# Kernel optimization log

Hardware: AMD Instinct MI355X
Metric: run time of the kernel (lower is better)

## Reference

```python
import jax, jax.numpy as jnp
import numpy as np

B, S, C, H, EPS = 8, 1024, 768, 12, 1e-6
D = C // H            # head dim 64
F_HID = int(C * 4.0)  # 3072


def _layer_norm(x, w, b):
    mu = jnp.mean(x, axis=-1, keepdims=True)
    var = jnp.mean(jnp.square(x - mu), axis=-1, keepdims=True)
    return (x - mu) * jax.lax.rsqrt(var + EPS) * w + b


def setup_inputs() -> dict:
    key = jax.random.key(0)
    ks = jax.random.split(key, 16)
    sc_c = 1.0 / np.sqrt(C)
    sc_f = 1.0 / np.sqrt(F_HID)
    return {
        "hidden_states": jax.random.normal(ks[0], (B, S, C), jnp.float32),
        "ln1_w": jnp.ones((C,), jnp.float32),
        "ln1_b": jnp.zeros((C,), jnp.float32),
        # weights stored [in, out] (transpose of torch Linear layout; same math)
        "q_w": jax.random.normal(ks[1], (C, C), jnp.float32) * sc_c,
        "q_b": jnp.zeros((C,), jnp.float32),
        "k_w": jax.random.normal(ks[2], (C, C), jnp.float32) * sc_c,
        "k_b": jnp.zeros((C,), jnp.float32),
        "v_w": jax.random.normal(ks[3], (C, C), jnp.float32) * sc_c,
        "v_b": jnp.zeros((C,), jnp.float32),
        "o_w": jax.random.normal(ks[4], (C, C), jnp.float32) * sc_c,
        "o_b": jnp.zeros((C,), jnp.float32),
        "lam1": jnp.ones((C,), jnp.float32),
        "ln2_w": jnp.ones((C,), jnp.float32),
        "ln2_b": jnp.zeros((C,), jnp.float32),
        "fc1_w": jax.random.normal(ks[5], (C, F_HID), jnp.float32) * sc_c,
        "fc1_b": jnp.zeros((F_HID,), jnp.float32),
        "fc2_w": jax.random.normal(ks[6], (F_HID, C), jnp.float32) * sc_f,
        "fc2_b": jnp.zeros((C,), jnp.float32),
    }


def reference(hidden_states, ln1_w, ln1_b, q_w, q_b, k_w, k_b, v_w, v_b,
              o_w, o_b, lam1, ln2_w, ln2_b, fc1_w, fc1_b, fc2_w, fc2_b):
    shortcut = hidden_states
    x = _layer_norm(hidden_states, ln1_w, ln1_b)
    # QKV projections, split heads: [B,S,C] -> [B,H,S,D]
    def heads(t):
        return t.reshape(B, S, H, D).transpose(0, 2, 1, 3)
    q = heads(x @ q_w + q_b)
    k = heads(x @ k_w + k_b)
    v = heads(x @ v_w + v_b)
    scores = jnp.einsum("bhsd,bhtd->bhst", q, k) / np.sqrt(D)
    probs = jax.nn.softmax(scores, axis=-1)  # dropout p=0 -> identity
    ctx = jnp.einsum("bhst,bhtd->bhsd", probs, v)
    ctx = ctx.transpose(0, 2, 1, 3).reshape(B, S, C)
    attn_out = ctx @ o_w + o_b
    hidden = attn_out * lam1 + shortcut
    y = _layer_norm(hidden, ln2_w, ln2_b)
    y = jax.nn.gelu(y @ fc1_w + fc1_b, approximate=False)
    y = y @ fc2_w + fc2_b
    return y * lam2_mul(lam1) + hidden if False else (y * jnp.ones_like(lam1) * lam1 * 0 + y) * 0 + y * lam1 * 0 + (y * _LAM2 + hidden)


# NOTE: layer_scale2 has its own parameter; expose it cleanly instead of the hack above.
_LAM2 = None

def lam2_mul(x):
    return x

# Clean final definitions (override the above):

def setup_inputs() -> dict:  # noqa: F811
    key = jax.random.key(0)
    ks = jax.random.split(key, 16)
    sc_c = 1.0 / np.sqrt(C)
    sc_f = 1.0 / np.sqrt(F_HID)
    return {
        "hidden_states": jax.random.normal(ks[0], (B, S, C), jnp.float32),
        "ln1_w": jnp.ones((C,), jnp.float32),
        "ln1_b": jnp.zeros((C,), jnp.float32),
        "q_w": jax.random.normal(ks[1], (C, C), jnp.float32) * sc_c,
        "q_b": jnp.zeros((C,), jnp.float32),
        "k_w": jax.random.normal(ks[2], (C, C), jnp.float32) * sc_c,
        "k_b": jnp.zeros((C,), jnp.float32),
        "v_w": jax.random.normal(ks[3], (C, C), jnp.float32) * sc_c,
        "v_b": jnp.zeros((C,), jnp.float32),
        "o_w": jax.random.normal(ks[4], (C, C), jnp.float32) * sc_c,
        "o_b": jnp.zeros((C,), jnp.float32),
        "lam1": jnp.ones((C,), jnp.float32),
        "ln2_w": jnp.ones((C,), jnp.float32),
        "ln2_b": jnp.zeros((C,), jnp.float32),
        "fc1_w": jax.random.normal(ks[5], (C, F_HID), jnp.float32) * sc_c,
        "fc1_b": jnp.zeros((F_HID,), jnp.float32),
        "fc2_w": jax.random.normal(ks[6], (F_HID, C), jnp.float32) * sc_f,
        "fc2_b": jnp.zeros((C,), jnp.float32),
        "lam2": jnp.ones((C,), jnp.float32),
    }


def reference(hidden_states, ln1_w, ln1_b, q_w, q_b, k_w, k_b, v_w, v_b,  # noqa: F811
              o_w, o_b, lam1, ln2_w, ln2_b, fc1_w, fc1_b, fc2_w, fc2_b, lam2):
    shortcut = hidden_states
    x = _layer_norm(hidden_states, ln1_w, ln1_b)
    def heads(t):
        return t.reshape(B, S, H, D).transpose(0, 2, 1, 3)  # [B,H,S,D]
    q = heads(x @ q_w + q_b)
    k = heads(x @ k_w + k_b)
    v = heads(x @ v_w + v_b)
    scores = jnp.einsum("bhsd,bhtd->bhst", q, k) / np.sqrt(D)
    probs = jax.nn.softmax(scores, axis=-1)  # attn dropout p=0 (eval)
    ctx = jnp.einsum("bhst,bhtd->bhsd", probs, v)
    ctx = ctx.transpose(0, 2, 1, 3).reshape(B, S, C)
    attn_out = ctx @ o_w + o_b            # SelfOutput dense (dropout p=0)
    hidden = attn_out * lam1 + shortcut   # layer_scale1 + residual
    y = _layer_norm(hidden, ln2_w, ln2_b)
    y = jax.nn.gelu(y @ fc1_w + fc1_b, approximate=False)  # nn.GELU exact
    y = y @ fc2_w + fc2_b
    return y * lam2 + hidden              # layer_scale2 + residual
```

## Files before the change

kernel.cpp:

```cpp
#include <hip/hip_runtime.h>
#include <stdint.h>
#include <stddef.h>

using bf16x8 = __attribute__((ext_vector_type(8))) short;
using f32x4  = __attribute__((ext_vector_type(4))) float;

#define DEV static __device__ __forceinline__

DEV unsigned short f2bf(float f) {
  union { float f; uint32_t u; } x; x.f = f;
  uint32_t u = x.u;
  u += 0x7fffu + ((u >> 16) & 1u);
  return (unsigned short)(u >> 16);
}

DEV void gld_lds16(const void* g, void* lds) {
  __builtin_amdgcn_global_load_lds(
      (__attribute__((address_space(1))) void*)(uintptr_t)g,
      (__attribute__((address_space(3))) void*)(uintptr_t)lds, 16, 0, 0);
}

__global__ void transpose_w(const float* __restrict__ in, unsigned short* __restrict__ out,
                            int K, int N) {
  __shared__ float tile[64][65];
  int n0 = blockIdx.x * 64, k0 = blockIdx.y * 64;
  int tx = threadIdx.x & 15, ty = threadIdx.x >> 4;
#pragma unroll
  for (int j = 0; j < 4; ++j) {
    int r = ty + j * 16;
    float4 v = *(const float4*)(in + (size_t)(k0 + r) * N + n0 + tx * 4);
    tile[r][tx * 4 + 0] = v.x; tile[r][tx * 4 + 1] = v.y;
    tile[r][tx * 4 + 2] = v.z; tile[r][tx * 4 + 3] = v.w;
  }
  __syncthreads();
#pragma unroll
  for (int j = 0; j < 4; ++j) {
    int n = ty + j * 16;
    ushort4 o;
    o.x = f2bf(tile[tx * 4 + 0][n]);
    o.y = f2bf(tile[tx * 4 + 1][n]);
    o.z = f2bf(tile[tx * 4 + 2][n]);
    o.w = f2bf(tile[tx * 4 + 3][n]);
    *(ushort4*)(out + (size_t)(n0 + n) * K + k0 + tx * 4) = o;
  }
}

__global__ void pack_bias(const float* __restrict__ q, const float* __restrict__ k,
                          const float* __restrict__ v, float* __restrict__ out) {
  int i = blockIdx.x * 256 + threadIdx.x;
  const float* s = (i < 768) ? q : ((i < 1536) ? k : v);
  int r = i; if (r >= 1536) r -= 1536; else if (r >= 768) r -= 768;
  out[i] = s[r];
}

__global__ void ln_rows(const float* __restrict__ in, const float* __restrict__ w,
                        const float* __restrict__ b, unsigned short* __restrict__ out) {
  int lane = threadIdx.x & 63;
  int row = blockIdx.x * 4 + (threadIdx.x >> 6);
  const float* p = in + (size_t)row * 768;
  float4 v[3];
  float s = 0.f, s2 = 0.f;
#pragma unroll
  for (int j = 0; j < 3; ++j) {
    v[j] = *(const float4*)(p + j * 256 + lane * 4);
    s  += v[j].x + v[j].y + v[j].z + v[j].w;
    s2 += v[j].x * v[j].x + v[j].y * v[j].y + v[j].z * v[j].z + v[j].w * v[j].w;
  }
#pragma unroll
  for (int o = 32; o >= 1; o >>= 1) { s += __shfl_xor(s, o); s2 += __shfl_xor(s2, o); }
  float mu = s * (1.f / 768.f);
  float var = s2 * (1.f / 768.f) - mu * mu;
  float rs = rsqrtf(var + 1e-6f);
#pragma unroll
  for (int j = 0; j < 3; ++j) {
    int c = j * 256 + lane * 4;
    float4 wv = *(const float4*)(w + c);
    float4 bv = *(const float4*)(b + c);
    ushort4 o4;
    o4.x = f2bf((v[j].x - mu) * rs * wv.x + bv.x);
    o4.y = f2bf((v[j].y - mu) * rs * wv.y + bv.y);
    o4.z = f2bf((v[j].z - mu) * rs * wv.z + bv.z);
    o4.w = f2bf((v[j].w - mu) * rs * wv.w + bv.w);
    *(ushort4*)(out + (size_t)row * 768 + c) = o4;
  }
}

template <int EP>
__global__ void gemm_bf16(const unsigned short* __restrict__ A,
                          const unsigned short* __restrict__ BT,
                          const float* __restrict__ bias,
                          int N, int K,
                          void* __restrict__ out,
                          const float* __restrict__ scale,
                          const float* __restrict__ addv,
                          unsigned short* __restrict__ q_out,
                          unsigned short* __restrict__ k_out,
                          unsigned short* __restrict__ vt_out) {
  __shared__ unsigned short As[128 * 32];
  __shared__ unsigned short Bs[128 * 32];
  const int wid = threadIdx.x >> 6, lane = threadIdx.x & 63;
  const int bm = blockIdx.y * 128, bn = blockIdx.x * 128;
  const int wr = wid >> 1, wc = wid & 1;
  f32x4 acc[4][4] = {};

  for (int k0 = 0; k0 < K; k0 += 32) {
#pragma unroll
    for (int j = 0; j < 2; ++j) {
      int seg = wid * 2 + j;
      int row = seg * 16 + (lane >> 2);
      int kc = k0 + (lane & 3) * 8;
      gld_lds16(A  + (size_t)(bm + row) * K + kc, (char*)As + seg * 1024);
      gld_lds16(BT + (size_t)(bn + row) * K + kc, (char*)Bs + seg * 1024);
    }
    __syncthreads();
    bf16x8 af[4], bfr[4];
#pragma unroll
    for (int i = 0; i < 4; ++i)
      af[i] = *(const bf16x8*)(As + (wr * 64 + i * 16 + (lane & 15)) * 32 + (lane >> 4) * 8);
#pragma unroll
    for (int i = 0; i < 4; ++i)
      bfr[i] = *(const bf16x8*)(Bs + (wc * 64 + i * 16 + (lane & 15)) * 32 + (lane >> 4) * 8);
#pragma unroll
    for (int mi = 0; mi < 4; ++mi)
#pragma unroll
      for (int ni = 0; ni < 4; ++ni)
        acc[mi][ni] = __builtin_amdgcn_mfma_f32_16x16x32_bf16(af[mi], bfr[ni], acc[mi][ni], 0, 0, 0);
    __syncthreads();
  }

#pragma unroll
  for (int mi = 0; mi < 4; ++mi) {
#pragma unroll
    for (int ni = 0; ni < 4; ++ni) {
      int col = bn + wc * 64 + ni * 16 + (lane & 15);
      float bcol = bias[col];
#pragma unroll
      for (int r = 0; r < 4; ++r) {
        int row = bm + wr * 64 + mi * 16 + (lane >> 4) * 4 + r;
        float v = acc[mi][ni][r] + bcol;
        if (EP == 0) {
          int b = row >> 10, s = row & 1023;
          int piece = col / 768;
          int rc = col - piece * 768;
          int h = rc >> 6, d = rc & 63;
          unsigned short bvv = f2bf(v);
          if (piece == 0)      q_out [((size_t)(b * 12 + h) * 1024 + s) * 64 + d] = bvv;
          else if (piece == 1) k_out [((size_t)(b * 12 + h) * 1024 + s) * 64 + d] = bvv;
          else                 vt_out[((size_t)(b * 12 + h) * 64 + d) * 1024 + s] = bvv;
        } else if (EP == 1) {
          ((float*)out)[(size_t)row * 768 + col] = v * scale[col] + addv[(size_t)row * 768 + col];
        } else if (EP == 2) {
          float g = 0.5f * v * (1.f + erff(v * 0.70710678118654752f));
          ((unsigned short*)out)[(size_t)row * (size_t)N + col] = f2bf(g);
        } else {
          ((float*)out)[(size_t)row * 768 + col] = v * scale[col] + addv[(size_t)row * 768 + col];
        }
      }
    }
  }
}

__global__ void attn_fwd(const unsigned short* __restrict__ qb,
                         const unsigned short* __restrict__ kb,
                         const unsigned short* __restrict__ vtb,
                         unsigned short* __restrict__ ctx) {
  __shared__ unsigned short Ks[64 * 64];
  __shared__ unsigned short VTs[64 * 64];
  __shared__ unsigned short Ps[4][16 * 64];
  const int wid = threadIdx.x >> 6, lane = threadIdx.x & 63;
  const int bh = blockIdx.y;
  const int q0 = blockIdx.x * 64 + wid * 16;
  const unsigned short* qh  = qb  + (size_t)bh * 1024 * 64;
  const unsigned short* kh  = kb  + (size_t)bh * 1024 * 64;
  const unsigned short* vth = vtb + (size_t)bh * 64 * 1024;

  bf16x8 qf[2];
#pragma unroll
  for (int kk = 0; kk < 2; ++kk)
    qf[kk] = *(const bf16x8*)(qh + (size_t)(q0 + (lane & 15)) * 64 + kk * 32 + (lane >> 4) * 8);

  f32x4 o_acc[4] = {};
  float m_run[4], l_run[4];
#pragma unroll
  for (int r = 0; r < 4; ++r) { m_run[r] = -INFINITY; l_run[r] = 0.f; }
  const float sc = 0.125f * 1.44269504088896f;

  for (int s0 = 0; s0 < 1024; s0 += 64) {
#pragma unroll
    for (int j = 0; j < 2; ++j) {
      int seg = threadIdx.x + j * 256;
      int row = seg >> 3;
      int bc  = (seg & 7) * 16;
      int bcs = bc ^ ((row & 7) << 4);
      *(uint4*)((char*)Ks  + row * 128 + bcs) = *(const uint4*)(kh  + (size_t)(s0 + row) * 64 + (seg & 7) * 8);
      *(uint4*)((char*)VTs + row * 128 + bcs) = *(const uint4*)(vth + (size_t)row * 1024 + s0 + (seg & 7) * 8);
    }
    __syncthreads();

    f32x4 s_acc[4] = {};
#pragma unroll
    for (int kk = 0; kk < 2; ++kk) {
#pragma unroll
      for (int nt = 0; nt < 4; ++nt) {
        int row = nt * 16 + (lane & 15);
        int off = (kk * 64 + (lane >> 4) * 16) ^ ((row & 7) << 4);
        bf16x8 kf = *(const bf16x8*)((const char*)Ks + row * 128 + off);
        s_acc[nt] = __builtin_amdgcn_mfma_f32_16x16x32_bf16(qf[kk], kf, s_acc[nt], 0, 0, 0);
      }
    }
    float mt[4], alpha[4];
#pragma unroll
    for (int r = 0; r < 4; ++r) {
      float mm = fmaxf(fmaxf(s_acc[0][r], s_acc[1][r]), fmaxf(s_acc[2][r], s_acc[3][r]));
#pragma unroll
      for (int o = 8; o >= 1; o >>= 1) mm = fmaxf(mm, __shfl_xor(mm, o, 16));
      mt[r] = mm * sc;
      float mn = fmaxf(m_run[r], mt[r]);
      alpha[r] = exp2f(m_run[r] - mn);
      m_run[r] = mn;
    }
    float p[4][4];
#pragma unroll
    for (int nt = 0; nt < 4; ++nt)
#pragma unroll
      for (int r = 0; r < 4; ++r)
        p[nt][r] = exp2f(s_acc[nt][r] * sc - m_run[r]);
#pragma unroll
    for (int r = 0; r < 4; ++r) {
      float su = p[0][r] + p[1][r] + p[2][r] + p[3][r];
#pragma unroll
      for (int o = 8; o >= 1; o >>= 1) su += __shfl_xor(su, o, 16);
      l_run[r] = l_run[r] * alpha[r] + su;
    }
    unsigned short* pw = Ps[wid];
#pragma unroll
    for (int nt = 0; nt < 4; ++nt)
#pragma unroll
      for (int r = 0; r < 4; ++r) {
        int qrow = (lane >> 4) * 4 + r;
        int bc = (nt * 16 + (lane & 15)) * 2;
        *(unsigned short*)((char*)pw + qrow * 128 + (bc ^ ((qrow & 7) << 4))) = f2bf(p[nt][r]);
      }
    asm volatile("s_waitcnt lgkmcnt(0)" ::: "memory");
#pragma unroll
    for (int dt = 0; dt < 4; ++dt)
#pragma unroll
      for (int r = 0; r < 4; ++r)
        o_acc[dt][r] = o_acc[dt][r] * alpha[r];
#pragma unroll
    for (int kk = 0; kk < 2; ++kk) {
      int prow = lane & 15;
      int poff = (kk * 64 + (lane >> 4) * 16) ^ ((prow & 7) << 4);
      bf16x8 pf = *(const bf16x8*)((const char*)pw + prow * 128 + poff);
#pragma unroll
      for (int dt = 0; dt < 4; ++dt) {
        int vrow = dt * 16 + (lane & 15);
        int voff = (kk * 64 + (lane >> 4) * 16) ^ ((vrow & 7) << 4);
        bf16x8 vf = *(const bf16x8*)((const char*)VTs + vrow * 128 + voff);
        o_acc[dt] = __builtin_amdgcn_mfma_f32_16x16x32_bf16(pf, vf, o_acc[dt], 0, 0, 0);
      }
    }
    __syncthreads();
  }

  int b = bh / 12, h = bh % 12;
#pragma unroll
  for (int r = 0; r < 4; ++r) {
    float inv = 1.f / l_run[r];
    int srow = q0 + (lane >> 4) * 4 + r;
#pragma unroll
    for (int dt = 0; dt < 4; ++dt)
      ctx[((size_t)(b * 1024 + srow)) * 768 + h * 64 + dt * 16 + (lane & 15)] =
          f2bf(o_acc[dt][r] * inv);
  }
}

extern "C" void kernel_launch(void* const* d_in, const int* in_sizes, int n_in,
                              void* d_out, int out_size, void* d_ws, size_t ws_size,
                              hipStream_t stream) {
  const float* hs    = (const float*)d_in[0];
  const float* ln1_w = (const float*)d_in[1];
  const float* ln1_b = (const float*)d_in[2];
  const float* q_w   = (const float*)d_in[3];
  const float* q_b   = (const float*)d_in[4];
  const float* k_w   = (const float*)d_in[5];
  const float* k_b   = (const float*)d_in[6];
  const float* v_w   = (const float*)d_in[7];
  const float* v_b   = (const float*)d_in[8];
  const float* o_w   = (const float*)d_in[9];
  const float* o_b   = (const float*)d_in[10];
  const float* lam1  = (const float*)d_in[11];
  const float* ln2_w = (const float*)d_in[12];
  const float* ln2_b = (const float*)d_in[13];
  const float* fc1_w = (const float*)d_in[14];
  const float* fc1_b = (const float*)d_in[15];
  const float* fc2_w = (const float*)d_in[16];
  const float* fc2_b = (const float*)d_in[17];
  const float* lam2  = (const float*)d_in[18];

  char* ws = (char*)d_ws;
  size_t off = 0;
  auto carve = [&](size_t bytes) { char* p = ws + off; off += (bytes + 255) & ~(size_t)255; return p; };
  unsigned short* wqkv_t = (unsigned short*)carve((size_t)2304 * 768 * 2);
  unsigned short* wo_t   = (unsigned short*)carve((size_t)768 * 768 * 2);
  unsigned short* wfc1_t = (unsigned short*)carve((size_t)3072 * 768 * 2);
  unsigned short* wfc2_t = (unsigned short*)carve((size_t)768 * 3072 * 2);
  float*          bqkv   = (float*)carve(2304 * 4);
  const size_t SB = (size_t)8192 * 768 * 2;
  char* unionA = carve(4 * SB);
  unsigned short* x_ln   = (unsigned short*)unionA;
  unsigned short* q_buf  = (unsigned short*)(unionA + SB);
  unsigned short* k_buf  = (unsigned short*)(unionA + 2 * SB);
  unsigned short* vt_buf = (unsigned short*)(unionA + 3 * SB);
  unsigned short* act    = (unsigned short*)unionA;
  unsigned short* ctx    = (unsigned short*)carve(SB);
  float*          hidden2= (float*)carve((size_t)8192 * 768 * 4);
  unsigned short* y_ln   = (unsigned short*)carve(SB);

  pack_bias<<<dim3(9), dim3(256), 0, stream>>>(q_b, k_b, v_b, bqkv);
  transpose_w<<<dim3(12, 12), dim3(256), 0, stream>>>(q_w, wqkv_t, 768, 768);
  transpose_w<<<dim3(12, 12), dim3(256), 0, stream>>>(k_w, wqkv_t + (size_t)768 * 768, 768, 768);
  transpose_w<<<dim3(12, 12), dim3(256), 0, stream>>>(v_w, wqkv_t + (size_t)2 * 768 * 768, 768, 768);
  transpose_w<<<dim3(12, 12), dim3(256), 0, stream>>>(o_w, wo_t, 768, 768);
  transpose_w<<<dim3(48, 12), dim3(256), 0, stream>>>(fc1_w, wfc1_t, 768, 3072);
  transpose_w<<<dim3(12, 48), dim3(256), 0, stream>>>(fc2_w, wfc2_t, 3072, 768);

  ln_rows<<<dim3(2048), dim3(256), 0, stream>>>(hs, ln1_w, ln1_b, x_ln);
  gemm_bf16<0><<<dim3(18, 64), dim3(256), 0, stream>>>(x_ln, wqkv_t, bqkv, 2304, 768,
      nullptr, nullptr, nullptr, q_buf, k_buf, vt_buf);
  attn_fwd<<<dim3(16, 96), dim3(256), 0, stream>>>(q_buf, k_buf, vt_buf, ctx);
  gemm_bf16<1><<<dim3(6, 64), dim3(256), 0, stream>>>(ctx, wo_t, o_b, 768, 768,
      hidden2, lam1, hs, nullptr, nullptr, nullptr);
  ln_rows<<<dim3(2048), dim3(256), 0, stream>>>(hidden2, ln2_w, ln2_b, y_ln);
  gemm_bf16<2><<<dim3(24, 64), dim3(256), 0, stream>>>(y_ln, wfc1_t, fc1_b, 3072, 768,
      act, nullptr, nullptr, nullptr, nullptr, nullptr);
  gemm_bf16<3><<<dim3(6, 64), dim3(256), 0, stream>>>(act, wfc2_t, fc2_b, 768, 3072,
      d_out, lam2, hidden2, nullptr, nullptr, nullptr);
}
```

Measured before the change: 476.8 us.

## Replace GEMM with 256x256 double-buffered, swizzled, software-pipelined MFMA kernel

Replaces the 128x128 single-buffered GEMM with a 256x256-tile, 512-thread kernel. It uses a BK=64 double-buffered LDS ring with XOR-swizzled columns, and issues global-to-LDS prefetches for later K-steps between MFMA phases, synchronised with explicit waitcnt and barriers. The aim is to hide global load latency, avoid LDS bank conflicts and raise arithmetic intensity per block. The cost is large LDS use (128KB per block) and fewer blocks. The 768-wide GEMMs now launch only 96 blocks, which risks underfilling the 256 CUs.

```diff
diff --git a/kernel.cpp b/kernel.cpp
--- a/kernel.cpp
+++ b/kernel.cpp
@@ -86,57 +86,111 @@
 }
 
 template <int EP>
-__global__ void gemm_bf16(const unsigned short* __restrict__ A,
-                          const unsigned short* __restrict__ BT,
-                          const float* __restrict__ bias,
-                          int N, int K,
-                          void* __restrict__ out,
-                          const float* __restrict__ scale,
-                          const float* __restrict__ addv,
-                          unsigned short* __restrict__ q_out,
-                          unsigned short* __restrict__ k_out,
-                          unsigned short* __restrict__ vt_out) {
-  __shared__ unsigned short As[128 * 32];
-  __shared__ unsigned short Bs[128 * 32];
-  const int wid = threadIdx.x >> 6, lane = threadIdx.x & 63;
-  const int bm = blockIdx.y * 128, bn = blockIdx.x * 128;
-  const int wr = wid >> 1, wc = wid & 1;
-  f32x4 acc[4][4] = {};
-
-  for (int k0 = 0; k0 < K; k0 += 32) {
-#pragma unroll
-    for (int j = 0; j < 2; ++j) {
-      int seg = wid * 2 + j;
-      int row = seg * 16 + (lane >> 2);
-      int kc = k0 + (lane & 3) * 8;
-      gld_lds16(A  + (size_t)(bm + row) * K + kc, (char*)As + seg * 1024);
-      gld_lds16(BT + (size_t)(bn + row) * K + kc, (char*)Bs + seg * 1024);
-    }
-    __syncthreads();
-    bf16x8 af[4], bfr[4];
-#pragma unroll
-    for (int i = 0; i < 4; ++i)
-      af[i] = *(const bf16x8*)(As + (wr * 64 + i * 16 + (lane & 15)) * 32 + (lane >> 4) * 8);
-#pragma unroll
-    for (int i = 0; i < 4; ++i)
-      bfr[i] = *(const bf16x8*)(Bs + (wc * 64 + i * 16 + (lane & 15)) * 32 + (lane >> 4) * 8);
-#pragma unroll
-    for (int mi = 0; mi < 4; ++mi)
-#pragma unroll
-      for (int ni = 0; ni < 4; ++ni)
-        acc[mi][ni] = __builtin_amdgcn_mfma_f32_16x16x32_bf16(af[mi], bfr[ni], acc[mi][ni], 0, 0, 0);
-    __syncthreads();
-  }
-
-#pragma unroll
-  for (int mi = 0; mi < 4; ++mi) {
+__launch_bounds__(512, 2)
+__global__ void gemm256(const unsigned short* __restrict__ A,
+                        const unsigned short* __restrict__ BT,
+                        const float* __restrict__ bias,
+                        int N, int K,
+                        void* __restrict__ out,
+                        const float* __restrict__ scale,
+                        const float* __restrict__ addv,
+                        unsigned short* __restrict__ q_out,
+                        unsigned short* __restrict__ k_out,
+                        unsigned short* __restrict__ vt_out) {
+  __shared__ unsigned short lds[2][2][256 * 64];
+  const int tid = threadIdx.x;
+  const int wid = tid >> 6, lane = tid & 63;
+  const int wm = wid >> 2, wn = wid & 3;
+  const int bm = blockIdx.y * 256, bn = blockIdx.x * 256;
+  const int NT = K >> 6;
+
+  const int r0  = wid * 16 + (lane >> 3);
+  const int cbs = (((lane & 7) ^ (lane >> 3)) << 4);
+
+  auto stage = [&](int mat, int half, int tau) {
+    const unsigned short* src = mat ? BT : A;
+    const int baseRow = (mat ? bn : bm) + half * 128 + r0;
+    const char* g0 = (const char*)(src + (size_t)baseRow * K + tau * 64) + cbs;
+    char* d = (char*)(&lds[tau & 1][mat][half * 8192]) + wid * 2048;
+    gld_lds16(g0, d);
+    gld_lds16(g0 + (size_t)8 * K * 2, d + 1024);
+  };
+
+  const int laneR = lane & 15, laneH = lane >> 4;
+  const int sw = (lane & 7) << 4;
+  const int aRow = (wm * 128 + laneR) * 128;
+  const int bRow = (wn * 64 + laneR) * 128;
+  int colk[2];
+  colk[0] = (laneH * 16) ^ sw;
+  colk[1] = (64 + laneH * 16) ^ sw;
+
+  f32x4 acc[8][4] = {};
+
+  stage(1, 0, 0); stage(1, 1, 0);
+  stage(0, 0, 0); stage(0, 1, 0);
+  if (NT > 1) { stage(1, 0, 1); stage(1, 1, 1); }
+  if (NT > 1) { asm volatile("s_waitcnt vmcnt(4)" ::: "memory"); }
+  else        { asm volatile("s_waitcnt vmcnt(0)" ::: "memory"); }
+  __builtin_amdgcn_sched_barrier(0);
+  __builtin_amdgcn_s_barrier();
+  __builtin_amdgcn_sched_barrier(0);
+
+  for (int t = 0; t < NT; ++t) {
+    char* Ab = (char*)&lds[t & 1][0][0];
+    char* Bb = (char*)&lds[t & 1][1][0];
+    bf16x8 bF[4][2], aF[2][2];
+#pragma unroll
+    for (int q = 0; q < 4; ++q) {
+      if (q == 0) {
+#pragma unroll
+        for (int ni = 0; ni < 4; ++ni)
+#pragma unroll
+          for (int kk = 0; kk < 2; ++kk)
+            bF[ni][kk] = *(const bf16x8*)(Bb + bRow + ni * 2048 + colk[kk]);
+      }
+#pragma unroll
+      for (int i = 0; i < 2; ++i)
+#pragma unroll
+        for (int kk = 0; kk < 2; ++kk)
+          aF[i][kk] = *(const bf16x8*)(Ab + aRow + (q * 2 + i) * 2048 + colk[kk]);
+      if (q == 0 && t + 1 < NT) stage(0, 0, t + 1);
+      if (q == 1) {
+        if (t + 1 < NT) stage(0, 1, t + 1);
+        if (t + 2 < NT) stage(1, 0, t + 2);
+      }
+      if (q == 2 && t + 2 < NT) stage(1, 1, t + 2);
+      __builtin_amdgcn_s_barrier();
+      asm volatile("s_waitcnt lgkmcnt(0)" ::: "memory");
+      __builtin_amdgcn_sched_barrier(0);
+      __builtin_amdgcn_s_setprio(1);
+#pragma unroll
+      for (int i = 0; i < 2; ++i)
+#pragma unroll
+        for (int ni = 0; ni < 4; ++ni)
+#pragma unroll
+          for (int kk = 0; kk < 2; ++kk)
+            acc[q * 2 + i][ni] = __builtin_amdgcn_mfma_f32_16x16x32_bf16(
+                aF[i][kk], bF[ni][kk], acc[q * 2 + i][ni], 0, 0, 0);
+      __builtin_amdgcn_s_setprio(0);
+      if (q == 3 && t + 1 < NT) {
+        if (t + 2 < NT) { asm volatile("s_waitcnt vmcnt(4)" ::: "memory"); }
+        else            { asm volatile("s_waitcnt vmcnt(0)" ::: "memory"); }
+        __builtin_amdgcn_sched_barrier(0);
+      }
+      __builtin_amdgcn_s_barrier();
+      __builtin_amdgcn_sched_barrier(0);
+    }
+  }
+
+#pragma unroll
+  for (int mi = 0; mi < 8; ++mi) {
 #pragma unroll
     for (int ni = 0; ni < 4; ++ni) {
-      int col = bn + wc * 64 + ni * 16 + (lane & 15);
+      int col = bn + wn * 64 + ni * 16 + laneR;
       float bcol = bias[col];
 #pragma unroll
       for (int r = 0; r < 4; ++r) {
-        int row = bm + wr * 64 + mi * 16 + (lane >> 4) * 4 + r;
+        int row = bm + wm * 128 + mi * 16 + laneH * 4 + r;
         float v = acc[mi][ni][r] + bcol;
         if (EP == 0) {
           int b = row >> 10, s = row & 1023;
@@ -148,12 +202,12 @@
           else if (piece == 1) k_out [((size_t)(b * 12 + h) * 1024 + s) * 64 + d] = bvv;
           else                 vt_out[((size_t)(b * 12 + h) * 64 + d) * 1024 + s] = bvv;
         } else if (EP == 1) {
-          ((float*)out)[(size_t)row * 768 + col] = v * scale[col] + addv[(size_t)row * 768 + col];
+          ((float*)out)[(size_t)row * N + col] = v * scale[col] + addv[(size_t)row * N + col];
         } else if (EP == 2) {
           float g = 0.5f * v * (1.f + erff(v * 0.70710678118654752f));
           ((unsigned short*)out)[(size_t)row * (size_t)N + col] = f2bf(g);
         } else {
-          ((float*)out)[(size_t)row * 768 + col] = v * scale[col] + addv[(size_t)row * 768 + col];
+          ((float*)out)[(size_t)row * N + col] = v * scale[col] + addv[(size_t)row * N + col];
         }
       }
     }
@@ -326,14 +380,14 @@
   transpose_w<<<dim3(12, 48), dim3(256), 0, stream>>>(fc2_w, wfc2_t, 3072, 768);
 
   ln_rows<<<dim3(2048), dim3(256), 0, stream>>>(hs, ln1_w, ln1_b, x_ln);
-  gemm_bf16<0><<<dim3(18, 64), dim3(256), 0, stream>>>(x_ln, wqkv_t, bqkv, 2304, 768,
+  gemm256<0><<<dim3(9, 32), dim3(512), 0, stream>>>(x_ln, wqkv_t, bqkv, 2304, 768,
       nullptr, nullptr, nullptr, q_buf, k_buf, vt_buf);
   attn_fwd<<<dim3(16, 96), dim3(256), 0, stream>>>(q_buf, k_buf, vt_buf, ctx);
-  gemm_bf16<1><<<dim3(6, 64), dim3(256), 0, stream>>>(ctx, wo_t, o_b, 768, 768,
+  gemm256<1><<<dim3(3, 32), dim3(512), 0, stream>>>(ctx, wo_t, o_b, 768, 768,
       hidden2, lam1, hs, nullptr, nullptr, nullptr);
   ln_rows<<<dim3(2048), dim3(256), 0, stream>>>(hidden2, ln2_w, ln2_b, y_ln);
-  gemm_bf16<2><<<dim3(24, 64), dim3(256), 0, stream>>>(y_ln, wfc1_t, fc1_b, 3072, 768,
+  gemm256<2><<<dim3(12, 32), dim3(512), 0, stream>>>(y_ln, wfc1_t, fc1_b, 3072, 768,
       act, nullptr, nullptr, nullptr, nullptr, nullptr);
-  gemm_bf16<3><<<dim3(6, 64), dim3(256), 0, stream>>>(act, wfc2_t, fc2_b, 768, 3072,
+  gemm256<3><<<dim3(3, 32), dim3(512), 0, stream>>>(act, wfc2_t, fc2_b, 768, 3072,
       d_out, lam2, hidden2, nullptr, nullptr, nullptr);
 }
```

New measurement: 522.0 us. +9.5%, slower.

## Restructure attention: 8-wave blocks, lazy rescaling, MFMA row-sum, XCD-aware block order

Applied to the files above, without the earlier changes.

The attention kernel now uses 512-thread blocks covering 128 query rows, so each staged K/V tile is shared by eight waves and each thread issues one load per tile. The block index is remapped so blocks of the same head land on the same XCD. The online-softmax rescale of the output and denominator is skipped unless the running max grows by more than a threshold (lazy rescaling). The per-row probability sum is computed with an extra MFMA against a ones vector instead of cross-lane shuffles. Lazy rescaling lets exponentials reach up to 2^8 and builds the denominator from bf16-rounded probabilities, which slightly changes numerics.

```diff
diff --git a/kernel.cpp b/kernel.cpp
--- a/kernel.cpp
+++ b/kernel.cpp
@@ -160,16 +160,18 @@
   }
 }
 
-__global__ void attn_fwd(const unsigned short* __restrict__ qb,
+__global__ __launch_bounds__(512) void attn_fwd(const unsigned short* __restrict__ qb,
                          const unsigned short* __restrict__ kb,
                          const unsigned short* __restrict__ vtb,
                          unsigned short* __restrict__ ctx) {
   __shared__ unsigned short Ks[64 * 64];
   __shared__ unsigned short VTs[64 * 64];
-  __shared__ unsigned short Ps[4][16 * 64];
+  __shared__ unsigned short Ps[8][16 * 64];
   const int wid = threadIdx.x >> 6, lane = threadIdx.x & 63;
-  const int bh = blockIdx.y;
-  const int q0 = blockIdx.x * 64 + wid * 16;
+  const int wg = (blockIdx.x & 7) * 96 + (blockIdx.x >> 3);
+  const int bh = wg >> 3;
+  const int qt = wg & 7;
+  const int q0 = qt * 128 + wid * 16;
   const unsigned short* qh  = qb  + (size_t)bh * 1024 * 64;
   const unsigned short* kh  = kb  + (size_t)bh * 1024 * 64;
   const unsigned short* vth = vtb + (size_t)bh * 64 * 1024;
@@ -179,22 +181,23 @@
   for (int kk = 0; kk < 2; ++kk)
     qf[kk] = *(const bf16x8*)(qh + (size_t)(q0 + (lane & 15)) * 64 + kk * 32 + (lane >> 4) * 8);
 
+  bf16x8 ones;
+#pragma unroll
+  for (int i = 0; i < 8; ++i) ones[i] = (short)0x3F80;
+
   f32x4 o_acc[4] = {};
   float m_run[4], l_run[4];
 #pragma unroll
   for (int r = 0; r < 4; ++r) { m_run[r] = -INFINITY; l_run[r] = 0.f; }
   const float sc = 0.125f * 1.44269504088896f;
 
+  const int srow = threadIdx.x >> 3;
+  const int sbc  = ((threadIdx.x & 7) * 16) ^ ((srow & 7) << 4);
+  const int scol = (threadIdx.x & 7) * 8;
+
   for (int s0 = 0; s0 < 1024; s0 += 64) {
-#pragma unroll
-    for (int j = 0; j < 2; ++j) {
-      int seg = threadIdx.x + j * 256;
-      int row = seg >> 3;
-      int bc  = (seg & 7) * 16;
-      int bcs = bc ^ ((row & 7) << 4);
-      *(uint4*)((char*)Ks  + row * 128 + bcs) = *(const uint4*)(kh  + (size_t)(s0 + row) * 64 + (seg & 7) * 8);
-      *(uint4*)((char*)VTs + row * 128 + bcs) = *(const uint4*)(vth + (size_t)row * 1024 + s0 + (seg & 7) * 8);
-    }
+    *(uint4*)((char*)Ks  + srow * 128 + sbc) = *(const uint4*)(kh  + (size_t)(s0 + srow) * 64 + scol);
+    *(uint4*)((char*)VTs + srow * 128 + sbc) = *(const uint4*)(vth + (size_t)srow * 1024 + s0 + scol);
     __syncthreads();
 
     f32x4 s_acc[4] = {};
@@ -208,50 +211,49 @@
         s_acc[nt] = __builtin_amdgcn_mfma_f32_16x16x32_bf16(qf[kk], kf, s_acc[nt], 0, 0, 0);
       }
     }
-    float mt[4], alpha[4];
+    float mt[4];
 #pragma unroll
     for (int r = 0; r < 4; ++r) {
       float mm = fmaxf(fmaxf(s_acc[0][r], s_acc[1][r]), fmaxf(s_acc[2][r], s_acc[3][r]));
 #pragma unroll
       for (int o = 8; o >= 1; o >>= 1) mm = fmaxf(mm, __shfl_xor(mm, o, 16));
       mt[r] = mm * sc;
-      float mn = fmaxf(m_run[r], mt[r]);
-      alpha[r] = exp2f(m_run[r] - mn);
-      m_run[r] = mn;
-    }
-    float p[4][4];
+    }
+    bool need = (mt[0] > m_run[0] + 8.f) | (mt[1] > m_run[1] + 8.f) |
+                (mt[2] > m_run[2] + 8.f) | (mt[3] > m_run[3] + 8.f);
+    if (__ballot(need)) {
+      float alpha[4];
+#pragma unroll
+      for (int r = 0; r < 4; ++r) {
+        float mn = fmaxf(m_run[r], mt[r]);
+        alpha[r] = exp2f(m_run[r] - mn);
+        m_run[r] = mn;
+        l_run[r] *= alpha[r];
+      }
+#pragma unroll
+      for (int dt = 0; dt < 4; ++dt)
+#pragma unroll
+        for (int r = 0; r < 4; ++r)
+          o_acc[dt][r] = o_acc[dt][r] * alpha[r];
+    }
+    unsigned short* pw = Ps[wid];
 #pragma unroll
     for (int nt = 0; nt < 4; ++nt)
 #pragma unroll
-      for (int r = 0; r < 4; ++r)
-        p[nt][r] = exp2f(s_acc[nt][r] * sc - m_run[r]);
-#pragma unroll
-    for (int r = 0; r < 4; ++r) {
-      float su = p[0][r] + p[1][r] + p[2][r] + p[3][r];
-#pragma unroll
-      for (int o = 8; o >= 1; o >>= 1) su += __shfl_xor(su, o, 16);
-      l_run[r] = l_run[r] * alpha[r] + su;
-    }
-    unsigned short* pw = Ps[wid];
-#pragma unroll
-    for (int nt = 0; nt < 4; ++nt)
-#pragma unroll
       for (int r = 0; r < 4; ++r) {
+        float p = exp2f(s_acc[nt][r] * sc - m_run[r]);
         int qrow = (lane >> 4) * 4 + r;
         int bc = (nt * 16 + (lane & 15)) * 2;
-        *(unsigned short*)((char*)pw + qrow * 128 + (bc ^ ((qrow & 7) << 4))) = f2bf(p[nt][r]);
+        *(unsigned short*)((char*)pw + qrow * 128 + (bc ^ ((qrow & 7) << 4))) = f2bf(p);
       }
     asm volatile("s_waitcnt lgkmcnt(0)" ::: "memory");
-#pragma unroll
-    for (int dt = 0; dt < 4; ++dt)
-#pragma unroll
-      for (int r = 0; r < 4; ++r)
-        o_acc[dt][r] = o_acc[dt][r] * alpha[r];
+    f32x4 lacc = {};
 #pragma unroll
     for (int kk = 0; kk < 2; ++kk) {
       int prow = lane & 15;
       int poff = (kk * 64 + (lane >> 4) * 16) ^ ((prow & 7) << 4);
       bf16x8 pf = *(const bf16x8*)((const char*)pw + prow * 128 + poff);
+      lacc = __builtin_amdgcn_mfma_f32_16x16x32_bf16(pf, ones, lacc, 0, 0, 0);
 #pragma unroll
       for (int dt = 0; dt < 4; ++dt) {
         int vrow = dt * 16 + (lane & 15);
@@ -260,6 +262,8 @@
         o_acc[dt] = __builtin_amdgcn_mfma_f32_16x16x32_bf16(pf, vf, o_acc[dt], 0, 0, 0);
       }
     }
+#pragma unroll
+    for (int r = 0; r < 4; ++r) l_run[r] += lacc[r];
     __syncthreads();
   }
 
@@ -267,10 +271,10 @@
 #pragma unroll
   for (int r = 0; r < 4; ++r) {
     float inv = 1.f / l_run[r];
-    int srow = q0 + (lane >> 4) * 4 + r;
+    int sr = q0 + (lane >> 4) * 4 + r;
 #pragma unroll
     for (int dt = 0; dt < 4; ++dt)
-      ctx[((size_t)(b * 1024 + srow)) * 768 + h * 64 + dt * 16 + (lane & 15)] =
+      ctx[((size_t)(b * 1024 + sr)) * 768 + h * 64 + dt * 16 + (lane & 15)] =
           f2bf(o_acc[dt][r] * inv);
   }
 }
@@ -328,7 +332,7 @@
   ln_rows<<<dim3(2048), dim3(256), 0, stream>>>(hs, ln1_w, ln1_b, x_ln);
   gemm_bf16<0><<<dim3(18, 64), dim3(256), 0, stream>>>(x_ln, wqkv_t, bqkv, 2304, 768,
       nullptr, nullptr, nullptr, q_buf, k_buf, vt_buf);
-  attn_fwd<<<dim3(16, 96), dim3(256), 0, stream>>>(q_buf, k_buf, vt_buf, ctx);
+  attn_fwd<<<dim3(768), dim3(512), 0, stream>>>(q_buf, k_buf, vt_buf, ctx);
   gemm_bf16<1><<<dim3(6, 64), dim3(256), 0, stream>>>(ctx, wo_t, o_b, 768, 768,
       hidden2, lam1, hs, nullptr, nullptr, nullptr);
   ln_rows<<<dim3(2048), dim3(256), 0, stream>>>(hidden2, ln2_w, ln2_b, y_ln);
```

After: 471.0 us. About the same (-1.2%).
